# Performance work log

Measured on AMD Instinct MI355X. Metric: run time of the kernel, lower is better.

The kernel has to match this reference:

```python
import jax, jax.numpy as jnp
import numpy as np

B, T, D = 2, 4096, 1024
HQ, HKV, HD = 16, 4, 64   # 16 query heads, 4 KV heads (kv_groups=4), head_dim=64
WIN = 256                 # sliding window radius (left == right == 256)


def setup_inputs() -> dict:
    key = jax.random.key(0)
    ks = jax.random.split(key, 9)
    s = 0.02  # small init scale for stable softmax logits
    return {
        "x": jax.random.normal(ks[0], (B, T, D), jnp.float32),
        "wq": jax.random.normal(ks[1], (D, HQ * HD), jnp.float32) * s,
        "bq": jnp.zeros((HQ * HD,), jnp.float32),
        "wk": jax.random.normal(ks[2], (D, HKV * HD), jnp.float32) * s,
        "bk": jnp.zeros((HKV * HD,), jnp.float32),
        "wv": jax.random.normal(ks[3], (D, HKV * HD), jnp.float32) * s,
        "bv": jnp.zeros((HKV * HD,), jnp.float32),
        "wo": jax.random.normal(ks[4], (HQ * HD, D), jnp.float32) * s,
        "bo": jnp.zeros((D,), jnp.float32),
    }


def _banded_gqa(q, k, v, left, right):
    """Sliding-window GQA attention: query i attends keys in [i-left, i+right].
    Never materializes the full [B,H,T,T] score matrix; uses banded blocks."""
    Bq, Tq, Hq, d = q.shape
    Hkv = k.shape[2]
    G = Hq // Hkv                      # query heads per KV head
    bs = max(left, right)              # block size == window radius; T % bs == 0
    nb = Tq // bs
    # queries: [B, nb, bs, Hkv, G, d]
    qb = q.reshape(Bq, nb, bs, Hkv, G, d)
    # gather 3 neighboring key/value blocks per query block (pad one block each side)
    pad = ((0, 0), (bs, bs), (0, 0), (0, 0))
    idx = jnp.arange(nb)[:, None] * bs + jnp.arange(3 * bs)[None, :]  # into padded seq
    kctx = jnp.pad(k, pad)[:, idx]     # [B, nb, 3bs, Hkv, d]
    vctx = jnp.pad(v, pad)[:, idx]     # [B, nb, 3bs, Hkv, d]
    scale = 1.0 / jnp.sqrt(jnp.asarray(d, q.dtype))
    # banded scores: [B, nb, Hkv, G, bs, 3bs]
    scores = jnp.einsum('bnqhgd,bnkhd->bnhgqk', qb, kctx) * scale
    qpos = jnp.arange(nb)[:, None, None] * bs + jnp.arange(bs)[None, :, None]
    kpos = (jnp.arange(nb)[:, None, None] - 1) * bs + jnp.arange(3 * bs)[None, None, :]
    valid = (kpos >= 0) & (kpos < Tq) & (kpos >= qpos - left) & (kpos <= qpos + right)
    scores = jnp.where(valid[None, :, None, None, :, :], scores, jnp.asarray(-1e30, scores.dtype))
    p = jax.nn.softmax(scores, axis=-1)
    out = jnp.einsum('bnhgqk,bnkhd->bnqhgd', p, vctx)
    return out.reshape(Bq, Tq, Hq, d)


def reference(x, wq, bq, wk, bk, wv, bv, wo, bo):
    q = (x @ wq + bq).reshape(B, T, HQ, HD)
    k = (x @ wk + bk).reshape(B, T, HKV, HD)
    v = (x @ wv + bv).reshape(B, T, HKV, HD)
    y = _banded_gqa(q, k, v, WIN, WIN)       # [B, T, HQ, HD]
    y = y.reshape(B, T, HQ * HD)
    return y @ wo + bo                        # dropout=0.0, deterministic -> identity
```

## Files before the change

kernel.cpp:

```cpp
#include <hip/hip_runtime.h>

typedef unsigned short u16;
typedef u16 u16x4 __attribute__((ext_vector_type(4)));
typedef u16 u16x8 __attribute__((ext_vector_type(8)));
typedef __bf16 bf16x8 __attribute__((ext_vector_type(8)));
typedef float f32x4 __attribute__((ext_vector_type(4)));

#define DEVINL static __device__ __forceinline__

DEVINL u16 f2bf(float f) {
    unsigned u = __builtin_bit_cast(unsigned, f);
    u += 0x7fff + ((u >> 16) & 1);
    return (u16)(u >> 16);
}

DEVINL f32x4 mfma_bf16(u16x8 a, u16x8 b, f32x4 c) {
    return __builtin_amdgcn_mfma_f32_16x16x32_bf16(
        __builtin_bit_cast(bf16x8, a), __builtin_bit_cast(bf16x8, b), c, 0, 0, 0);
}

DEVINL void gload16(const void* g, void* lds) {
    __builtin_amdgcn_global_load_lds(
        (const __attribute__((address_space(1))) void*)g,
        (__attribute__((address_space(3))) void*)lds, 16, 0, 0);
}


__global__ void cvt_x_kernel(const float4* __restrict__ x4, u16x4* __restrict__ o4) {
    int idx = blockIdx.x * 256 + threadIdx.x;
    float4 a = x4[idx];
    u16x4 o;
    o[0] = f2bf(a.x); o[1] = f2bf(a.y); o[2] = f2bf(a.z); o[3] = f2bf(a.w);
    o4[idx] = o;
}

__global__ void fill_bias(const float* __restrict__ bq, const float* __restrict__ bk,
                          const float* __restrict__ bv, float* __restrict__ dst) {
    int i = blockIdx.x * 256 + threadIdx.x;
    if (i < 1024) dst[i] = bq[i];
    else if (i < 1280) dst[i] = bk[i - 1024];
    else if (i < 1536) dst[i] = bv[i - 1280];
}

__global__ void twt_kernel(const float* __restrict__ src, u16* __restrict__ dst,
                           int N, int rowOff) {
    __shared__ float t[64][65];
    int k0 = blockIdx.x * 64, n0 = blockIdx.y * 64;
    int tid = threadIdx.x;
#pragma unroll
    for (int j = 0; j < 16; j++) {
        int idx = j * 256 + tid; int r = idx >> 6, c = idx & 63;
        t[r][c] = src[(size_t)(k0 + r) * N + n0 + c];
    }
    __syncthreads();
#pragma unroll
    for (int j = 0; j < 16; j++) {
        int idx = j * 256 + tid; int r = idx >> 6, c = idx & 63;
        dst[(size_t)(rowOff + n0 + r) * 1024 + k0 + c] = f2bf(t[c][r]);
    }
}

__global__ void tv_kernel(const u16* __restrict__ qkv, u16* __restrict__ vt) {
    __shared__ u16 t[64][68];
    int t0 = blockIdx.x * 64; int h = blockIdx.y; int b = blockIdx.z;
    int tid = threadIdx.x;
#pragma unroll
    for (int j = 0; j < 16; j++) {
        int idx = j * 256 + tid; int r = idx >> 6, c = idx & 63;
        t[r][c] = qkv[(size_t)(b * 4096 + t0 + r) * 1536 + 1280 + h * 64 + c];
    }
    __syncthreads();
#pragma unroll
    for (int j = 0; j < 16; j++) {
        int idx = j * 256 + tid; int r = idx >> 6, c = idx & 63;
        vt[(size_t)((b * 4 + h) * 64 + r) * 4096 + t0 + c] = t[c][r];
    }
}


template <bool F32OUT>
__global__ __launch_bounds__(256, 2) void gemm_bt(
    const u16* __restrict__ A, const u16* __restrict__ Bt, void* __restrict__ Cp,
    const float* __restrict__ bias, int M, int N, int K) {
    __shared__ __align__(16) u16 As[128 * 64];
    __shared__ __align__(16) u16 Bs[128 * 64];
    int tid = threadIdx.x; int l = tid & 63; int w = tid >> 6;
    int m0 = blockIdx.y * 128, n0 = blockIdx.x * 128;
    int wm = (w >> 1) * 64, wn = (w & 1) * 64;
    f32x4 acc[4][4] = {};

    int srow[4], scol[4];
#pragma unroll
    for (int c = 0; c < 4; c++) {
        int b = (w * 4 + c) * 1024 + l * 16;
        int row = b >> 7, inner = b & 127;
        srow[c] = row;
        scol[c] = (inner ^ ((row & 7) << 4)) >> 1;
    }
    int nk = K >> 6;
    for (int kt = 0; kt < nk; ++kt) {
        int kb = kt << 6;
#pragma unroll
        for (int c = 0; c < 4; c++) {
            gload16(A + (size_t)(m0 + srow[c]) * K + kb + scol[c], (char*)As + (w * 4 + c) * 1024);
            gload16(Bt + (size_t)(n0 + srow[c]) * K + kb + scol[c], (char*)Bs + (w * 4 + c) * 1024);
        }
        __syncthreads();
#pragma unroll
        for (int kc = 0; kc < 2; ++kc) {
            int co = (kc * 32 + (l >> 4) * 8) * 2;
            u16x8 af[4], bf[4];
#pragma unroll
            for (int mf = 0; mf < 4; ++mf) {
                int row = wm + mf * 16 + (l & 15);
                af[mf] = *(const u16x8*)((const char*)As + row * 128 + (co ^ ((row & 7) << 4)));
            }
#pragma unroll
            for (int nf = 0; nf < 4; ++nf) {
                int row = wn + nf * 16 + (l & 15);
                bf[nf] = *(const u16x8*)((const char*)Bs + row * 128 + (co ^ ((row & 7) << 4)));
            }
#pragma unroll
            for (int mf = 0; mf < 4; ++mf)
#pragma unroll
                for (int nf = 0; nf < 4; ++nf)
                    acc[mf][nf] = mfma_bf16(af[mf], bf[nf], acc[mf][nf]);
        }
        __syncthreads();
    }
#pragma unroll
    for (int mf = 0; mf < 4; ++mf) {
#pragma unroll
        for (int nf = 0; nf < 4; ++nf) {
            int col = n0 + wn + nf * 16 + (l & 15);
            float bv = bias ? bias[col] : 0.0f;
#pragma unroll
            for (int r = 0; r < 4; r++) {
                int row = m0 + wm + mf * 16 + (l >> 4) * 4 + r;
                float v = acc[mf][nf][r] + bv;
                if (F32OUT) ((float*)Cp)[(size_t)row * N + col] = v;
                else        ((u16*)Cp)[(size_t)row * N + col] = f2bf(v);
            }
        }
    }
}


#define SCALE2 0.18033688f

__global__ __launch_bounds__(512, 4) void attn_kernel(
    const u16* __restrict__ qkv, const u16* __restrict__ vt, u16* __restrict__ y) {
    __shared__ __align__(16) u16 Ks[64 * 64];
    __shared__ __align__(16) u16 Vs[64 * 64];
    __shared__ __align__(16) u16 Ps[8][32 * 64];
    int tid = threadIdx.x, l = tid & 63, w = tid >> 6;
    int head = w >> 1, qh = w & 1;
    int qb = blockIdx.x, h = blockIdx.y, b = blockIdx.z;
    int qstart = qb * 64;
    size_t rowbase = (size_t)b * 4096;
    int hq = h * 4 + head;

    u16x8 qf_[2][2];
#pragma unroll
    for (int qf = 0; qf < 2; ++qf)
#pragma unroll
        for (int kc = 0; kc < 2; ++kc)
            qf_[qf][kc] = *(const u16x8*)(qkv + (rowbase + qstart + qh * 32 + qf * 16 + (l & 15)) * 1536
                                          + hq * 64 + kc * 32 + (l >> 4) * 8);

    f32x4 o[2][4] = {};
    float mrow[2], srow_[2];
#pragma unroll
    for (int i = 0; i < 2; i++) { mrow[i] = -__builtin_inff(); srow_[i] = 0.f; }

    const u16* kbase_ptr = qkv + 1024 + h * 64;
    const u16* vbase_ptr = vt + (size_t)((b * 4 + h) * 64) * 4096;

    int sb_ = w * 1024 + l * 16;
    int g_row = sb_ >> 7, g_inner = sb_ & 127;
    int g_col = (g_inner ^ ((g_row & 7) << 4)) >> 1;

    for (int kstart = qstart - 256; kstart <= qstart + 256; kstart += 64) {
        if (kstart < 0 || kstart >= 4096) continue;
        gload16(kbase_ptr + (rowbase + kstart + g_row) * 1536 + g_col, (char*)Ks + w * 1024);
        gload16(vbase_ptr + (size_t)g_row * 4096 + kstart + g_col, (char*)Vs + w * 1024);
        __syncthreads();

        f32x4 st[4][2] = {};
#pragma unroll
        for (int kc = 0; kc < 2; ++kc) {
            int co = (kc * 32 + (l >> 4) * 8) * 2;
            u16x8 kf_[4];
#pragma unroll
            for (int kf = 0; kf < 4; ++kf) {
                int row = kf * 16 + (l & 15);
                kf_[kf] = *(const u16x8*)((const char*)Ks + row * 128 + (co ^ ((row & 7) << 4)));
            }
#pragma unroll
            for (int kf = 0; kf < 4; ++kf)
#pragma unroll
                for (int qf = 0; qf < 2; ++qf)
                    st[kf][qf] = mfma_bf16(kf_[kf], qf_[qf][kc], st[kf][qf]);
        }

        bool mlo = (kstart == qstart - 256);
        bool mhi = (kstart == qstart + 256);

#pragma unroll
        for (int qf = 0; qf < 2; ++qf) {
            int qoff = qh * 32 + qf * 16 + (l & 15);
            float pmax = -1e30f;
            float sv[4][4];
#pragma unroll
            for (int kf = 0; kf < 4; ++kf)
#pragma unroll
                for (int r = 0; r < 4; r++) {
                    int koff = kf * 16 + (l >> 4) * 4 + r;
                    float v = st[kf][qf][r] * SCALE2;
                    if (mlo && koff < qoff) v = -1e30f;
                    if (mhi && koff > qoff) v = -1e30f;
                    sv[kf][r] = v;
                    pmax = fmaxf(pmax, v);
                }
            pmax = fmaxf(pmax, __shfl_xor(pmax, 16));
            pmax = fmaxf(pmax, __shfl_xor(pmax, 32));

            bool resc = !__all(pmax - mrow[qf] <= 8.0f);
            float newm = resc ? fmaxf(mrow[qf], pmax) : mrow[qf];
            float psum = 0.f;
#pragma unroll
            for (int kf = 0; kf < 4; ++kf) {
                u16x4 pk;
#pragma unroll
                for (int r = 0; r < 4; r++) {
                    float e = __builtin_amdgcn_exp2f(sv[kf][r] - newm);
                    psum += e;
                    pk[r] = f2bf(e);
                }
                int row = qf * 16 + (l & 15);
                int keyc = kf * 16 + (l >> 4) * 4;
                *(u16x4*)((char*)Ps[w] + ((row * 128 + keyc * 2) ^ ((row & 7) << 4))) = pk;
            }
            psum += __shfl_xor(psum, 16);
            psum += __shfl_xor(psum, 32);
            if (resc) {
                float fs = __builtin_amdgcn_exp2f(mrow[qf] - newm);
                srow_[qf] = srow_[qf] * fs + psum;
                mrow[qf] = newm;
#pragma unroll
                for (int r = 0; r < 4; r++) {
                    float fb = __shfl(fs, (l >> 4) * 4 + r);
#pragma unroll
                    for (int nf = 0; nf < 4; ++nf) o[qf][nf][r] *= fb;
                }
            } else {
                srow_[qf] += psum;
            }
        }

#pragma unroll
        for (int kc = 0; kc < 2; ++kc) {
            int co = (kc * 32 + (l >> 4) * 8) * 2;
            u16x8 vb[4];
#pragma unroll
            for (int nf = 0; nf < 4; ++nf) {
                int row = nf * 16 + (l & 15);
                vb[nf] = *(const u16x8*)((const char*)Vs + row * 128 + (co ^ ((row & 7) << 4)));
            }
#pragma unroll
            for (int mf = 0; mf < 2; ++mf) {
                int row = mf * 16 + (l & 15);
                u16x8 pa = *(const u16x8*)((const char*)Ps[w] + ((row * 128 + co) ^ ((row & 7) << 4)));
#pragma unroll
                for (int nf = 0; nf < 4; ++nf)
                    o[mf][nf] = mfma_bf16(pa, vb[nf], o[mf][nf]);
            }
        }
        __syncthreads();
    }

#pragma unroll
    for (int mf = 0; mf < 2; ++mf) {
        float inv = 1.0f / srow_[mf];
#pragma unroll
        for (int r = 0; r < 4; r++) {
            float sb = __shfl(inv, (l >> 4) * 4 + r);
            int row = qstart + qh * 32 + mf * 16 + (l >> 4) * 4 + r;
#pragma unroll
            for (int nf = 0; nf < 4; ++nf) {
                int col = hq * 64 + nf * 16 + (l & 15);
                y[(rowbase + row) * 1024 + col] = f2bf(o[mf][nf][r] * sb);
            }
        }
    }
}


extern "C" void kernel_launch(void* const* d_in, const int* in_sizes, int n_in,
                              void* d_out, int out_size, void* d_ws, size_t ws_size,
                              hipStream_t stream) {
    const float* x  = (const float*)d_in[0];
    const float* wq = (const float*)d_in[1];
    const float* bq = (const float*)d_in[2];
    const float* wk = (const float*)d_in[3];
    const float* bk = (const float*)d_in[4];
    const float* wv = (const float*)d_in[5];
    const float* bv = (const float*)d_in[6];
    const float* wo = (const float*)d_in[7];
    const float* bo = (const float*)d_in[8];
    float* out = (float*)d_out;

    char* p = (char*)d_ws;
    u16* xb     = (u16*)p;   p += (size_t)8192 * 1024 * 2;
    u16* wqkvt  = (u16*)p;   p += (size_t)1536 * 1024 * 2;
    u16* wot    = (u16*)p;   p += (size_t)1024 * 1024 * 2;
    float* bqkv = (float*)p; p += 8192;
    u16* qkvb   = (u16*)p;   p += (size_t)8192 * 1536 * 2;
    u16* vtb    = (u16*)p;   p += (size_t)512 * 4096 * 2;
    u16* yb     = (u16*)p;

    cvt_x_kernel<<<8192, 256, 0, stream>>>((const float4*)x, (u16x4*)xb);
    fill_bias<<<6, 256, 0, stream>>>(bq, bk, bv, bqkv);
    twt_kernel<<<dim3(16, 16), 256, 0, stream>>>(wq, wqkvt, 1024, 0);
    twt_kernel<<<dim3(16, 4),  256, 0, stream>>>(wk, wqkvt, 256, 1024);
    twt_kernel<<<dim3(16, 4),  256, 0, stream>>>(wv, wqkvt, 256, 1280);
    twt_kernel<<<dim3(16, 16), 256, 0, stream>>>(wo, wot, 1024, 0);

    gemm_bt<false><<<dim3(12, 64), 256, 0, stream>>>(xb, wqkvt, qkvb, bqkv, 8192, 1536, 1024);
    tv_kernel<<<dim3(64, 4, 2), 256, 0, stream>>>(qkvb, vtb);
    attn_kernel<<<dim3(64, 4, 2), 512, 0, stream>>>(qkvb, vtb, yb);
    gemm_bt<true><<<dim3(8, 64), 256, 0, stream>>>(yb, wot, out, bo, 8192, 1024, 1024);
}
```

Baseline: 128.7 us.

## Double-buffer K/V tiles in attention and fold softmax scale into Q projection

The attention kernel now double-buffers K and V tiles in LDS, prefetching the next tile with async global-to-LDS loads while computing the current one, and syncs with manual waitcnt and barriers. The softmax scale is applied to Q in the QKV GEMM epilogue instead of per score, and P is converted to bf16 with a cheaper rounding that does not handle ties to even. Query blocks are also remapped across the grid. This aims to hide load latency and remove per-score multiplies, at the cost of doubled K/V LDS and slightly different rounding of Q and P.

```diff
diff --git a/kernel.cpp b/kernel.cpp
--- a/kernel.cpp
+++ b/kernel.cpp
@@ -12,6 +12,11 @@
     unsigned u = __builtin_bit_cast(unsigned, f);
     u += 0x7fff + ((u >> 16) & 1);
     return (u16)(u >> 16);
+}
+
+DEVINL u16 pbf(float f) {
+    unsigned u = __builtin_bit_cast(unsigned, f);
+    return (u16)((u + 0x8000) >> 16);
 }
 
 DEVINL f32x4 mfma_bf16(u16x8 a, u16x8 b, f32x4 c) {
@@ -81,7 +86,7 @@
 template <bool F32OUT>
 __global__ __launch_bounds__(256, 2) void gemm_bt(
     const u16* __restrict__ A, const u16* __restrict__ Bt, void* __restrict__ Cp,
-    const float* __restrict__ bias, int M, int N, int K) {
+    const float* __restrict__ bias, int M, int N, int K, int qn, float qscale) {
     __shared__ __align__(16) u16 As[128 * 64];
     __shared__ __align__(16) u16 Bs[128 * 64];
     int tid = threadIdx.x; int l = tid & 63; int w = tid >> 6;
@@ -134,10 +139,11 @@
         for (int nf = 0; nf < 4; ++nf) {
             int col = n0 + wn + nf * 16 + (l & 15);
             float bv = bias ? bias[col] : 0.0f;
+            float scl = (col < qn) ? qscale : 1.0f;
 #pragma unroll
             for (int r = 0; r < 4; r++) {
                 int row = m0 + wm + mf * 16 + (l >> 4) * 4 + r;
-                float v = acc[mf][nf][r] + bv;
+                float v = (acc[mf][nf][r] + bv) * scl;
                 if (F32OUT) ((float*)Cp)[(size_t)row * N + col] = v;
                 else        ((u16*)Cp)[(size_t)row * N + col] = f2bf(v);
             }
@@ -146,16 +152,15 @@
 }
 
 
-#define SCALE2 0.18033688f
-
 __global__ __launch_bounds__(512, 4) void attn_kernel(
     const u16* __restrict__ qkv, const u16* __restrict__ vt, u16* __restrict__ y) {
-    __shared__ __align__(16) u16 Ks[64 * 64];
-    __shared__ __align__(16) u16 Vs[64 * 64];
+    __shared__ __align__(16) u16 Ks[2][64 * 64];
+    __shared__ __align__(16) u16 Vs[2][64 * 64];
     __shared__ __align__(16) u16 Ps[8][32 * 64];
     int tid = threadIdx.x, l = tid & 63, w = tid >> 6;
     int head = w >> 1, qh = w & 1;
-    int qb = blockIdx.x, h = blockIdx.y, b = blockIdx.z;
+    int qb = ((blockIdx.x & 7) << 3) | (blockIdx.x >> 3);
+    int h = blockIdx.y, b = blockIdx.z;
     int qstart = qb * 64;
     size_t rowbase = (size_t)b * 4096;
     int hq = h * 4 + head;
@@ -180,11 +185,31 @@
     int g_row = sb_ >> 7, g_inner = sb_ & 127;
     int g_col = (g_inner ^ ((g_row & 7) << 4)) >> 1;
 
-    for (int kstart = qstart - 256; kstart <= qstart + 256; kstart += 64) {
-        if (kstart < 0 || kstart >= 4096) continue;
-        gload16(kbase_ptr + (rowbase + kstart + g_row) * 1536 + g_col, (char*)Ks + w * 1024);
-        gload16(vbase_ptr + (size_t)g_row * 4096 + kstart + g_col, (char*)Vs + w * 1024);
-        __syncthreads();
+    int klo = qstart - 256; if (klo < 0) klo = 0;
+    int khi = qstart + 256; if (khi > 4096 - 64) khi = 4096 - 64;
+    int nt = ((khi - klo) >> 6) + 1;
+
+#define STAGE(bufi, ks_)                                                                  \
+    do {                                                                                  \
+        gload16(kbase_ptr + (rowbase + (ks_) + g_row) * 1536 + g_col,                     \
+                (char*)Ks[bufi] + w * 1024);                                              \
+        gload16(vbase_ptr + (size_t)g_row * 4096 + (ks_) + g_col,                         \
+                (char*)Vs[bufi] + w * 1024);                                              \
+    } while (0)
+
+    STAGE(0, klo);
+    for (int t = 0; t < nt; ++t) {
+        int kstart = klo + (t << 6);
+        bool pref = (t + 1 < nt);
+        if (pref) {
+            STAGE((t + 1) & 1, kstart + 64);
+            asm volatile("s_waitcnt vmcnt(2)" ::: "memory");
+        } else {
+            asm volatile("s_waitcnt vmcnt(0)" ::: "memory");
+        }
+        __builtin_amdgcn_s_barrier();
+        const char* Kb = (const char*)Ks[t & 1];
+        const char* Vb = (const char*)Vs[t & 1];
 
         f32x4 st[4][2] = {};
 #pragma unroll
@@ -194,7 +219,7 @@
 #pragma unroll
             for (int kf = 0; kf < 4; ++kf) {
                 int row = kf * 16 + (l & 15);
-                kf_[kf] = *(const u16x8*)((const char*)Ks + row * 128 + (co ^ ((row & 7) << 4)));
+                kf_[kf] = *(const u16x8*)(Kb + row * 128 + (co ^ ((row & 7) << 4)));
             }
 #pragma unroll
             for (int kf = 0; kf < 4; ++kf)
@@ -216,7 +241,7 @@
 #pragma unroll
                 for (int r = 0; r < 4; r++) {
                     int koff = kf * 16 + (l >> 4) * 4 + r;
-                    float v = st[kf][qf][r] * SCALE2;
+                    float v = st[kf][qf][r];
                     if (mlo && koff < qoff) v = -1e30f;
                     if (mhi && koff > qoff) v = -1e30f;
                     sv[kf][r] = v;
@@ -235,7 +260,7 @@
                 for (int r = 0; r < 4; r++) {
                     float e = __builtin_amdgcn_exp2f(sv[kf][r] - newm);
                     psum += e;
-                    pk[r] = f2bf(e);
+                    pk[r] = pbf(e);
                 }
                 int row = qf * 16 + (l & 15);
                 int keyc = kf * 16 + (l >> 4) * 4;
@@ -265,7 +290,7 @@
 #pragma unroll
             for (int nf = 0; nf < 4; ++nf) {
                 int row = nf * 16 + (l & 15);
-                vb[nf] = *(const u16x8*)((const char*)Vs + row * 128 + (co ^ ((row & 7) << 4)));
+                vb[nf] = *(const u16x8*)(Vb + row * 128 + (co ^ ((row & 7) << 4)));
             }
 #pragma unroll
             for (int mf = 0; mf < 2; ++mf) {
@@ -276,8 +301,10 @@
                     o[mf][nf] = mfma_bf16(pa, vb[nf], o[mf][nf]);
             }
         }
-        __syncthreads();
-    }
+        asm volatile("s_waitcnt lgkmcnt(0)" ::: "memory");
+        __builtin_amdgcn_s_barrier();
+    }
+#undef STAGE
 
 #pragma unroll
     for (int mf = 0; mf < 2; ++mf) {
@@ -326,8 +353,10 @@
     twt_kernel<<<dim3(16, 4),  256, 0, stream>>>(wv, wqkvt, 256, 1280);
     twt_kernel<<<dim3(16, 16), 256, 0, stream>>>(wo, wot, 1024, 0);
 
-    gemm_bt<false><<<dim3(12, 64), 256, 0, stream>>>(xb, wqkvt, qkvb, bqkv, 8192, 1536, 1024);
+    gemm_bt<false><<<dim3(12, 64), 256, 0, stream>>>(xb, wqkvt, qkvb, bqkv,
+                                                     8192, 1536, 1024, 1024, 0.18033688f);
     tv_kernel<<<dim3(64, 4, 2), 256, 0, stream>>>(qkvb, vtb);
     attn_kernel<<<dim3(64, 4, 2), 512, 0, stream>>>(qkvb, vtb, yb);
-    gemm_bt<true><<<dim3(8, 64), 256, 0, stream>>>(yb, wot, out, bo, 8192, 1024, 1024);
-}
+    gemm_bt<true><<<dim3(8, 64), 256, 0, stream>>>(yb, wot, out, bo,
+                                                   8192, 1024, 1024, 0, 1.0f);
+}
```

After: 137.7 us. +7.0%, slower.
